# Optimization experiments

Measured on AMD Instinct MI355X. Metric: run time of the kernel, lower is better.

Reference implementation:

```python
import jax, jax.numpy as jnp
import numpy as np
from jax import lax

B, N, D_PTS = 8, 4096, 6
N_POINTS, N_SAMPLES, RADIUS = 1024, 32, 0.2
MLPS = [64, 64, 128]
BN_EPS = 1e-3  # keras BatchNormalization default epsilon


def safe_norm(diff, axis):
    # euclidean norm with a backward-safe sqrt (same forward values)
    sq = jnp.sum(diff * diff, axis=axis)
    pos = sq > 0
    return jnp.where(pos, jnp.sqrt(jnp.where(pos, sq, 1.0)), 0.0)


def setup_inputs() -> dict:
    key = jax.random.key(0)
    ks = jax.random.split(key, 2)
    xyz = jax.random.normal(ks[0], (B, N, 3), jnp.float32)
    points = jax.random.normal(ks[1], (B, N, D_PTS), jnp.float32)
    inp = {"xyz": xyz, "points": points}
    c_in = 3 + D_PTS
    for i, c_out in enumerate(MLPS):
        kw = jax.random.fold_in(key, 100 + i)
        inp[f"w{i}"] = jax.random.normal(kw, (c_in, c_out), jnp.float32) * (1.0 / np.sqrt(c_in))
        inp[f"b{i}"] = jnp.zeros((c_out,), jnp.float32)
        inp[f"g{i}"] = jnp.ones((c_out,), jnp.float32)
        inp[f"be{i}"] = jnp.zeros((c_out,), jnp.float32)
        c_in = c_out
    return inp


def fps(xyz, n_points):
    # farthest point sampling; original seeds with a random index, we use 0 deterministically
    b, n, _ = xyz.shape
    init_idx = jnp.zeros((b,), jnp.int32)
    mask0 = jnp.ones((b, n), xyz.dtype)
    def step(carry, _):
        mask, last = carry
        added = jnp.take_along_axis(xyz, last[:, None, None], axis=1)  # [B,1,D]
        dist = safe_norm(xyz - added, 2) * mask                        # [B,N]
        nxt = jnp.argmax(dist, axis=1).astype(jnp.int32)
        new_mask = jnp.minimum(dist * mask * 1e11, mask)
        return (new_mask, nxt), nxt
    _, ids = lax.scan(step, (mask0, init_idx), None, length=n_points - 1)
    return jnp.concatenate([init_idx[:, None], ids.T], axis=1)  # [B, n_points]


def gather_points(x, idx):
    # x: [B,N,C]; idx: [B,...] -> [B,...,C]
    b = x.shape[0]
    flat = idx.reshape(b, -1)
    out = jnp.take_along_axis(x, flat[..., None], axis=1)
    return out.reshape(idx.shape + (x.shape[-1],))


def query_ball(radius, n_samples, xyz, cent_xyz):
    # faithful to source: compares norm to radius**2 (source quirk), full argsort then slice
    diff = xyz[:, None, :, :] - cent_xyz[:, :, None, :]   # [B,n,N,3]
    dist = safe_norm(diff, 3)                              # [B,n,N]
    dist = jnp.minimum(dist, radius * radius)
    return jnp.argsort(dist, axis=2)[:, :, :n_samples]     # [B,n,n_samples]


def mlp_layer(h, w, b, g, be):
    # pointwise Dense + BatchNormalization (batch stats, axis=-1) + relu
    h = jnp.einsum('bnsc,cd->bnsd', h, w) + b
    mean = jnp.mean(h, axis=(0, 1, 2), keepdims=True)
    var = jnp.var(h, axis=(0, 1, 2), keepdims=True)
    h = g * (h - mean) * lax.rsqrt(var + BN_EPS) + be
    return jax.nn.relu(h)


def forward(xyz, points, params):
    cent_idx = fps(xyz, N_POINTS)                 # [B, n_points]
    cent_xyz = gather_points(xyz, cent_idx)       # [B, n_points, 3]
    group_idx = query_ball(RADIUS, N_SAMPLES, xyz, cent_xyz)  # [B, n_points, n_samples]
    group_xyz = gather_points(xyz, group_idx)     # [B, n_points, n_samples, 3]
    group_pts = gather_points(points, group_idx)  # [B, n_points, n_samples, D]
    h = jnp.concatenate([group_xyz, group_pts], axis=-1)
    for (w, b, g, be) in params:
        h = mlp_layer(h, w, b, g, be)
    return cent_xyz, jnp.max(h, axis=2)           # [B,n_points,3], [B,n_points,128]


def reference(xyz, points, w0, b0, g0, be0, w1, b1, g1, be1, w2, b2, g2, be2):
    params = [(w0, b0, g0, be0), (w1, b1, g1, be1), (w2, b2, g2, be2)]
    return forward(xyz, points, params)
```

## Files before the change

kernel.cpp:

```cpp
#include <hip/hip_runtime.h>

#define NPTS  4096
#define NB    8
#define NC    1024
#define NSAMP 32
#define DP    6
#define C0    9
#define C3    128
#define ROWS_TOT 262144

#define OFF_SS   (32ull<<10)
#define OFF_Y0   (16ull<<20)
#define OFF_Y1   (96ull<<20)
#define OFF_PSUM (168ull<<20)
#define OFF_PSQ  (172ull<<20)
#define OFF_GMX  (176ull<<20)
#define OFF_GMN  (180ull<<20)

typedef unsigned long long ull;
typedef float v2f __attribute__((ext_vector_type(2)));

__device__ __forceinline__ float sqdist_noc(float x, float y, float z,
                                            float cx, float cy, float cz) {
  #pragma clang fp contract(off)
  float dx = x - cx, dy = y - cy, dz = z - cz;
  return dx * dx + dy * dy + dz * dz;
}

template <int CTRL, int RM>
__device__ __forceinline__ float dpp_mov_f(float x) {
  int xi = __float_as_int(x);
  int r = __builtin_amdgcn_update_dpp(xi, xi, CTRL, RM, 0xf, false);
  return __int_as_float(r);
}

__device__ __forceinline__ float wave64_fmax(float x) {
  x = fmaxf(x, dpp_mov_f<0x111, 0xf>(x));
  x = fmaxf(x, dpp_mov_f<0x112, 0xf>(x));
  x = fmaxf(x, dpp_mov_f<0x114, 0xf>(x));
  x = fmaxf(x, dpp_mov_f<0x118, 0xf>(x));
  x = fmaxf(x, dpp_mov_f<0x142, 0xa>(x));
  x = fmaxf(x, dpp_mov_f<0x143, 0xc>(x));
  return x;
}

__global__ __launch_bounds__(256)
void fps_kernel(const float* __restrict__ xyz, float* __restrict__ cent) {
  const int b = blockIdx.x;
  const int t = threadIdx.x;
  const float* X = xyz + (size_t)b * NPTS * 3;
  float* OC = cent + (size_t)b * NC * 3;

  __shared__ float4 sxyz[NPTS];
  __shared__ float4 wkc[2][4];
  __shared__ alignas(16) int wki[2][4];
  __shared__ int sidx[NC];

  for (int p = t; p < NPTS; p += 256)
    sxyz[p] = make_float4(X[p * 3 + 0], X[p * 3 + 1], X[p * 3 + 2], 0.f);
  __syncthreads();

  float px[16], py[16], pz[16], h[16];
  #pragma unroll
  for (int i = 0; i < 16; i++) {
    float4 v = sxyz[t * 16 + i];
    px[i] = v.x; py[i] = v.y; pz[i] = v.z;
    h[i] = fmaf(v.x, v.x, fmaf(v.y, v.y, v.z * v.z));
  }

  const int wv = t >> 6;
  float4 c;

  auto step_body = [&](int pw_) {
    const float c2x = c.x + c.x, c2y = c.y + c.y, c2z = c.z + c.z;
    float key[16]; int idx[16];
    #pragma unroll
    for (int i = 0; i < 16; i++) {
      key[i] = fmaf(pz[i], -c2z, fmaf(py[i], -c2y, fmaf(px[i], -c2x, h[i])));
      idx[i] = i;
    }
    #pragma unroll
    for (int s = 1; s < 16; s <<= 1) {
      #pragma unroll
      for (int i = 0; i < 16; i += 2 * s) {
        bool tk = key[i + s] > key[i];
        key[i] = tk ? key[i + s] : key[i];
        idx[i] = tk ? idx[i + s] : idx[i];
      }
    }
    const float mx = key[0];
    const int mj = idx[0];
    float4 cand = sxyz[(t << 4) + mj];
    float wm = wave64_fmax(mx);
    float smax = __int_as_float(__builtin_amdgcn_readlane(__float_as_int(wm), 63));
    if (mx == smax) {
      wkc[pw_][wv] = make_float4(cand.x, cand.y, cand.z, smax);
      wki[pw_][wv] = (t << 4) + mj;
    }
  };

  auto fold = [&](int pr_) -> int {
    float4 q0 = wkc[pr_][0], q1 = wkc[pr_][1];
    float4 q2 = wkc[pr_][2], q3 = wkc[pr_][3];
    const int4 ii = *(const int4*)&wki[pr_][0];
    bool g1 = q1.w > q0.w; float4 ca = g1 ? q1 : q0; int ia = g1 ? ii.y : ii.x;
    bool g3 = q3.w > q2.w; float4 cb = g3 ? q3 : q2; int ib = g3 ? ii.w : ii.z;
    bool gb = cb.w > ca.w; c = gb ? cb : ca; return gb ? ib : ia;
  };

  if (t == 0) { sidx[0] = 0; h[0] = -__builtin_inff(); }
  c = sxyz[0];
  step_body(1);
  __syncthreads();

  for (int k = 2; k < NC; k++) {
    const int pr = (k - 1) & 1, pw = k & 1;
    int gidx = fold(pr);
    if (t == 0) sidx[k - 1] = gidx;
    if ((gidx >> 4) == t) {
      int m = gidx & 15;
      #pragma unroll
      for (int i = 0; i < 16; i++)
        if (i == m) h[i] = -__builtin_inff();
    }
    step_body(pw);
    __syncthreads();
  }
  {
    int gidx = fold(1023 & 1);
    if (t == 0) sidx[NC - 1] = gidx;
  }
  __syncthreads();
  for (int i = t; i < NC; i += 256) {
    float4 cc = sxyz[sidx[i]];
    OC[i * 3 + 0] = cc.x;
    OC[i * 3 + 1] = cc.y;
    OC[i * 3 + 2] = cc.z;
  }
}

#define BCAP 256
__global__ __launch_bounds__(256)
void ball_dense0_kernel(const float* __restrict__ xyz, const float* __restrict__ pts,
                        const float* __restrict__ cent,
                        const float* __restrict__ W0, const float* __restrict__ b0,
                        float* __restrict__ y0,
                        float* __restrict__ psum, float* __restrict__ psq) {
  const int blk = blockIdx.x;
  const int b = blk >> 10;
  const int t = threadIdx.x;
  const float* X = xyz + (size_t)b * NPTS * 3;
  const float* P = pts + (size_t)b * NPTS * DP;
  const float cx = cent[(size_t)blk * 3 + 0];
  const float cy = cent[(size_t)blk * 3 + 1];
  const float cz = cent[(size_t)blk * 3 + 2];

  __shared__ int scount;
  __shared__ ull skeys[BCAP];
  __shared__ ull ssorted[BCAP];
  __shared__ int sel[NSAMP];
  __shared__ float xs0[NSAMP * C0];
  __shared__ float w0s[C0 * 64];
  __shared__ float b0s[64];
  __shared__ float red[2][NSAMP][64];
  if (t == 0) scount = 0;
  for (int e = t; e < C0 * 64; e += 256) w0s[e] = W0[e];
  if (t < 64) b0s[t] = b0[t];
  __syncthreads();

  {
    float4 xb[12];
    const float4* Xv = (const float4*)(X + (size_t)t * 48);
    #pragma unroll
    for (int i = 0; i < 12; i++) xb[i] = Xv[i];
    const float* xf = (const float*)xb;
    v2f sq2[8];
    {
      #pragma clang fp contract(off)
      const v2f c2x = v2f{cx, cx}, c2y = v2f{cy, cy}, c2z = v2f{cz, cz};
      #pragma unroll
      for (int i = 0; i < 8; i++) {
        v2f x2 = v2f{xf[6 * i + 0], xf[6 * i + 3]};
        v2f y2 = v2f{xf[6 * i + 1], xf[6 * i + 4]};
        v2f z2 = v2f{xf[6 * i + 2], xf[6 * i + 5]};
        v2f dx = x2 - c2x, dy = y2 - c2y, dz = z2 - c2z;
        sq2[i] = (dx * dx + dy * dy) + dz * dz;
      }
    }
    #pragma unroll
    for (int i = 0; i < 16; i++) {
      int j = t * 16 + i;
      float sq = (i & 1) ? sq2[i >> 1].y : sq2[i >> 1].x;
      if (sq < 0.0017f) {
        float d = (sq > 0.f) ? sqrtf(sq) : 0.f;
        if (d < 0.04f) {
          int pos = atomicAdd(&scount, 1);
          if (pos < BCAP)
            skeys[pos] = ((ull)(unsigned)__float_as_int(d) << 12) | (unsigned)j;
        }
      }
    }
  }
  __syncthreads();
  const int M = min(scount, BCAP);

  if (t < M) {
    ull my = skeys[t];
    int r = 0;
    for (int j2 = 0; j2 < M; j2++) r += (skeys[j2] < my);
    ssorted[r] = my;
  }
  __syncthreads();

  if (t < NSAMP) {
    int v;
    if (t < M) {
      v = (int)(ssorted[t] & 0xFFFull);
    } else {
      int s = t - M;
      int idx = s;
      for (int it = 0; it < 40; it++) {
        int c = 0;
        for (int j2 = 0; j2 < M; j2++) c += ((int)(skeys[j2] & 0xFFFull) <= idx);
        int nidx = s + c;
        if (nidx == idx) break;
        idx = nidx;
      }
      v = idx;
    }
    sel[t] = v;
  }
  __syncthreads();

  for (int e = t; e < NSAMP * C0; e += 256) {
    int k = e / C0;
    int cc = e - k * C0;
    int j = sel[k];
    xs0[e] = (cc < 3) ? X[j * 3 + cc] : P[j * DP + (cc - 3)];
  }
  __syncthreads();

  const int row = t >> 3, c8 = (t & 7) * 8;
  float a[8];
  #pragma unroll
  for (int j = 0; j < 8; j++) a[j] = b0s[c8 + j];
  #pragma unroll
  for (int k = 0; k < C0; k++) {
    float xv = xs0[row * C0 + k];
    #pragma unroll
    for (int j = 0; j < 8; j++) a[j] = fmaf(xv, w0s[k * 64 + c8 + j], a[j]);
  }
  float* Y = y0 + ((size_t)blk * NSAMP + row) * 64 + c8;
  *(float4*)(Y + 0) = make_float4(a[0], a[1], a[2], a[3]);
  *(float4*)(Y + 4) = make_float4(a[4], a[5], a[6], a[7]);
  #pragma unroll
  for (int j = 0; j < 8; j++) red[0][row][c8 + j] = a[j];
  #pragma unroll
  for (int j = 0; j < 8; j++) red[1][row][c8 + j] = a[j] * a[j];
  __syncthreads();
  if (t < 64) {
    float S = 0.f, Q = 0.f;
    #pragma unroll
    for (int g = 0; g < NSAMP; g++) { S += red[0][g][t]; Q += red[1][g][t]; }
    psum[(size_t)t * 8192 + blk] = S;
    psq [(size_t)t * 8192 + blk] = Q;
  }
}

__global__ __launch_bounds__(256)
void dense_lane1_kernel(const float* __restrict__ y0, const float* __restrict__ ss0,
                        const float* __restrict__ W1, const float* __restrict__ b1,
                        float* __restrict__ y1,
                        float* __restrict__ psum, float* __restrict__ psq) {
  __shared__ float tr[4][64][33];
  __shared__ float wred[2][4][64];
  const int t = threadIdx.x, wid = t >> 6, lane = t & 63;
  const size_t row = (size_t)blockIdx.x * 256 + (size_t)(wid * 64 + lane);
  float acc[64];
  #pragma unroll
  for (int c = 0; c < 64; c++) acc[c] = b1[c];
  const float* Xr = y0 + row * 64;
  #pragma unroll 1
  for (int k0 = 0; k0 < 64; k0 += 4) {
    float4 xv = *(const float4*)(Xr + k0);
    #pragma unroll
    for (int kk = 0; kk < 4; kk++) {
      const int k = k0 + kk;
      float x = fmaxf(fmaf((&xv.x)[kk], ss0[k], ss0[128 + k]), 0.f);
      const float* Wk = W1 + k * 64;
      #pragma unroll
      for (int c = 0; c < 64; c++) acc[c] = fmaf(x, Wk[c], acc[c]);
    }
  }
  float* Yr = y1 + row * 64;
  #pragma unroll
  for (int c0 = 0; c0 < 64; c0 += 4)
    *(float4*)(Yr + c0) = make_float4(acc[c0], acc[c0 + 1], acc[c0 + 2], acc[c0 + 3]);
  const int c = lane & 31;
  const bool isQ = lane >= 32;
  #pragma unroll
  for (int chunk = 0; chunk < 2; chunk++) {
    __syncthreads();
    #pragma unroll
    for (int j = 0; j < 32; j++) tr[wid][lane][j] = acc[chunk * 32 + j];
    __syncthreads();
    float A = 0.f;
    for (int r = 0; r < 64; r++) {
      float v = tr[wid][r][c];
      A = fmaf(v, isQ ? v : 1.0f, A);
    }
    wred[isQ ? 1 : 0][wid][chunk * 32 + c] = A;
  }
  __syncthreads();
  if (t < 64) {
    float S = 0.f, Q = 0.f;
    #pragma unroll
    for (int w = 0; w < 4; w++) { S += wred[0][w][t]; Q += wred[1][w][t]; }
    psum[(size_t)t * 1024 + blockIdx.x] = S;
    psq [(size_t)t * 1024 + blockIdx.x] = Q;
  }
}

__global__ __launch_bounds__(256)
void dense_lane2_kernel(const float* __restrict__ y1, const float* __restrict__ ss1,
                        const float* __restrict__ W2, const float* __restrict__ b2,
                        float* __restrict__ psum, float* __restrict__ psq,
                        float* __restrict__ gmax, float* __restrict__ gmin) {
  __shared__ float tr[4][64][33];
  __shared__ float wred[2][4][128];
  const int t = threadIdx.x, wid = t >> 6, lane = t & 63;
  const size_t row = (size_t)blockIdx.x * 256 + (size_t)(wid * 64 + lane);
  const int centA = blockIdx.x * 8 + wid * 2;
  const int centB = centA + 1;

  float x[64];
  const float* Xr = y1 + row * 64;
  #pragma unroll
  for (int k0 = 0; k0 < 64; k0 += 4) {
    float4 xv = *(const float4*)(Xr + k0);
    #pragma unroll
    for (int kk = 0; kk < 4; kk++)
      x[k0 + kk] = fmaxf(fmaf((&xv.x)[kk], ss1[k0 + kk], ss1[128 + k0 + kk]), 0.f);
  }

  const int c = lane & 31;
  const bool isQ = lane >= 32;
  #pragma unroll 1
  for (int half = 0; half < 2; half++) {
    float acc[64];
    #pragma unroll
    for (int cc = 0; cc < 64; cc++) acc[cc] = b2[half * 64 + cc];
    #pragma unroll 1
    for (int k = 0; k < 64; k++) {
      const float* Wk = W2 + k * C3 + half * 64;
      const float xk = x[k];
      #pragma unroll
      for (int cc = 0; cc < 64; cc++) acc[cc] = fmaf(xk, Wk[cc], acc[cc]);
    }
    #pragma unroll
    for (int chunk = 0; chunk < 2; chunk++) {
      __syncthreads();
      #pragma unroll
      for (int j = 0; j < 32; j++) tr[wid][lane][j] = acc[chunk * 32 + j];
      __syncthreads();
      const int ch = half * 64 + chunk * 32 + c;
      float A = 0.f, m1 = -__builtin_inff(), m2 = -__builtin_inff();
      for (int r = 0; r < 32; r++) {
        float v = tr[wid][r][c];
        A = fmaf(v, isQ ? v : 1.0f, A);
        m1 = fmaxf(m1, isQ ? -v : v);
      }
      for (int r = 32; r < 64; r++) {
        float v = tr[wid][r][c];
        A = fmaf(v, isQ ? v : 1.0f, A);
        m2 = fmaxf(m2, isQ ? -v : v);
      }
      wred[isQ ? 1 : 0][wid][ch] = A;
      if (!isQ) {
        gmax[(size_t)centA * C3 + ch] = m1;
        gmax[(size_t)centB * C3 + ch] = m2;
      } else {
        gmin[(size_t)centA * C3 + ch] = -m1;
        gmin[(size_t)centB * C3 + ch] = -m2;
      }
    }
  }
  __syncthreads();
  if (t < C3) {
    float S = 0.f, Q = 0.f;
    #pragma unroll
    for (int w = 0; w < 4; w++) { S += wred[0][w][t]; Q += wred[1][w][t]; }
    psum[(size_t)t * 1024 + blockIdx.x] = S;
    psq [(size_t)t * 1024 + blockIdx.x] = Q;
  }
}

template <int NBLK>
__global__ __launch_bounds__(256)
void stats_final_kernel(const float* __restrict__ psum, const float* __restrict__ psq,
                        const float* __restrict__ g, const float* __restrict__ be,
                        float* __restrict__ ss_out) {
  const int c = blockIdx.x, t = threadIdx.x;
  float S = 0.f, Q = 0.f;
  for (int i = t; i < NBLK; i += 256) {
    S += psum[(size_t)c * NBLK + i];
    Q += psq [(size_t)c * NBLK + i];
  }
  __shared__ float sS[256], sQ[256];
  sS[t] = S; sQ[t] = Q;
  __syncthreads();
  #pragma unroll
  for (int off = 128; off; off >>= 1) {
    if (t < off) { sS[t] += sS[t + off]; sQ[t] += sQ[t + off]; }
    __syncthreads();
  }
  if (t == 0) {
    const float inv = 1.0f / 262144.0f;
    float mean = sS[0] * inv;
    float var = sQ[0] * inv - mean * mean;
    float scale = g[c] / sqrtf(var + 1e-3f);
    ss_out[c] = scale;
    ss_out[128 + c] = be[c] - mean * scale;
  }
}

__global__ __launch_bounds__(128)
void pool_final_kernel(const float* __restrict__ gmax, const float* __restrict__ gmin,
                       const float* __restrict__ ss2, float* __restrict__ out1) {
  const int blk = blockIdx.x, c = threadIdx.x;
  const float sc = ss2[c], sh = ss2[128 + c];
  float v = (sc >= 0.f) ? gmax[(size_t)blk * C3 + c] : gmin[(size_t)blk * C3 + c];
  out1[(size_t)blk * C3 + c] = fmaxf(fmaf(v, sc, sh), 0.f);
}

extern "C" void kernel_launch(void* const* d_in, const int* in_sizes, int n_in,
                              void* d_out, int out_size, void* d_ws, size_t ws_size,
                              hipStream_t stream) {
  const float* xyz = (const float*)d_in[0];
  const float* pts = (const float*)d_in[1];
  const float* w0 = (const float*)d_in[2];
  const float* b0 = (const float*)d_in[3];
  const float* g0 = (const float*)d_in[4];
  const float* be0 = (const float*)d_in[5];
  const float* w1 = (const float*)d_in[6];
  const float* b1 = (const float*)d_in[7];
  const float* g1 = (const float*)d_in[8];
  const float* be1 = (const float*)d_in[9];
  const float* w2 = (const float*)d_in[10];
  const float* b2 = (const float*)d_in[11];
  const float* g2 = (const float*)d_in[12];
  const float* be2 = (const float*)d_in[13];

  float* out = (float*)d_out;
  float* cent = out;
  float* out1 = out + (size_t)NB * NC * 3;

  char* ws = (char*)d_ws;
  float* ssA  = (float*)(ws + OFF_SS);
  float* y0   = (float*)(ws + OFF_Y0);
  float* y1   = (float*)(ws + OFF_Y1);
  float* psum = (float*)(ws + OFF_PSUM);
  float* psq  = (float*)(ws + OFF_PSQ);
  float* gmx  = (float*)(ws + OFF_GMX);
  float* gmn  = (float*)(ws + OFF_GMN);

  fps_kernel<<<dim3(NB), dim3(256), 0, stream>>>(xyz, cent);

  ball_dense0_kernel<<<dim3(NB * NC), dim3(256), 0, stream>>>(
      xyz, pts, cent, w0, b0, y0, psum, psq);
  stats_final_kernel<8192><<<dim3(64), dim3(256), 0, stream>>>(psum, psq, g0, be0, ssA + 0 * 256);

  dense_lane1_kernel<<<dim3(ROWS_TOT / 256), dim3(256), 0, stream>>>(
      y0, ssA + 0 * 256, w1, b1, y1, psum, psq);
  stats_final_kernel<1024><<<dim3(64), dim3(256), 0, stream>>>(psum, psq, g1, be1, ssA + 1 * 256);

  dense_lane2_kernel<<<dim3(ROWS_TOT / 256), dim3(256), 0, stream>>>(
      y1, ssA + 1 * 256, w2, b2, psum, psq, gmx, gmn);
  stats_final_kernel<1024><<<dim3(128), dim3(256), 0, stream>>>(psum, psq, g2, be2, ssA + 2 * 256);

  pool_final_kernel<<<dim3(NB * NC), dim3(128), 0, stream>>>(gmx, gmn, ssA + 2 * 256, out1);

  (void)in_sizes; (void)n_in; (void)out_size; (void)ws_size;
}
```

Measured before the change: 807.3 us.

## Fuse FPS and ball-query kernels with progress flags to overlap stages

Merges the farthest-point-sampling kernel and the ball-query/dense0 kernel into one persistent-style launch. Blocks take a ticket from an atomic counter: the first 8 run FPS and publish their progress every 32 centroids through release stores. The remaining blocks spin on that counter and start ball query and the first dense layer for each centroid as soon as it exists. This aims to hide the serial FPS latency behind the ball-query work, at the cost of spin-waiting blocks holding CU slots, an extra memset, and a shared-memory union that may lower occupancy.

```diff
diff --git a/kernel.cpp b/kernel.cpp
--- a/kernel.cpp
+++ b/kernel.cpp
@@ -20,13 +20,6 @@
 typedef unsigned long long ull;
 typedef float v2f __attribute__((ext_vector_type(2)));
 
-__device__ __forceinline__ float sqdist_noc(float x, float y, float z,
-                                            float cx, float cy, float cz) {
-  #pragma clang fp contract(off)
-  float dx = x - cx, dy = y - cy, dz = z - cz;
-  return dx * dx + dy * dy + dz * dz;
-}
-
 template <int CTRL, int RM>
 __device__ __forceinline__ float dpp_mov_f(float x) {
   int xi = __float_as_int(x);
@@ -44,226 +37,254 @@
   return x;
 }
 
+#define BCAP 256
+
+struct FpsShared {
+  float4 sxyz[NPTS];
+  float4 wkc[2][4];
+  int    wki[2][4];
+};
+struct BallShared {
+  ull skeys[BCAP];
+  ull ssorted[BCAP];
+  int sel[NSAMP];
+  float xs0[NSAMP * C0];
+  float w0s[C0 * 64];
+  float b0s[64];
+  float red[2][NSAMP][64];
+  float cbc[4];
+};
+
 __global__ __launch_bounds__(256)
-void fps_kernel(const float* __restrict__ xyz, float* __restrict__ cent) {
-  const int b = blockIdx.x;
+void fps_ball_kernel(const float* __restrict__ xyz, const float* __restrict__ pts,
+                     const float* __restrict__ W0, const float* __restrict__ b0v,
+                     float* __restrict__ cent, float* __restrict__ y0,
+                     float* __restrict__ psum, float* __restrict__ psq,
+                     int* __restrict__ ctl) {
+  __shared__ int s_tk;
+  __shared__ int s_cnt;
+  __shared__ alignas(16) unsigned char smem[sizeof(FpsShared)];
   const int t = threadIdx.x;
-  const float* X = xyz + (size_t)b * NPTS * 3;
-  float* OC = cent + (size_t)b * NC * 3;
-
-  __shared__ float4 sxyz[NPTS];
-  __shared__ float4 wkc[2][4];
-  __shared__ alignas(16) int wki[2][4];
-  __shared__ int sidx[NC];
-
-  for (int p = t; p < NPTS; p += 256)
-    sxyz[p] = make_float4(X[p * 3 + 0], X[p * 3 + 1], X[p * 3 + 2], 0.f);
+  if (t == 0) s_tk = atomicAdd(&ctl[0], 1);
   __syncthreads();
-
-  float px[16], py[16], pz[16], h[16];
-  #pragma unroll
-  for (int i = 0; i < 16; i++) {
-    float4 v = sxyz[t * 16 + i];
-    px[i] = v.x; py[i] = v.y; pz[i] = v.z;
-    h[i] = fmaf(v.x, v.x, fmaf(v.y, v.y, v.z * v.z));
-  }
-
-  const int wv = t >> 6;
-  float4 c;
-
-  auto step_body = [&](int pw_) {
-    const float c2x = c.x + c.x, c2y = c.y + c.y, c2z = c.z + c.z;
-    float key[16]; int idx[16];
+  const int tk = s_tk;
+
+  if (tk < NB) {
+    FpsShared& S = *reinterpret_cast<FpsShared*>(smem);
+    const int b = tk;
+    const float* X = xyz + (size_t)b * NPTS * 3;
+    float* OC = cent + (size_t)b * NC * 3;
+    int* prog = ctl + 16 + 16 * b;
+
+    for (int p = t; p < NPTS; p += 256)
+      S.sxyz[p] = make_float4(X[p * 3 + 0], X[p * 3 + 1], X[p * 3 + 2], 0.f);
+    __syncthreads();
+
+    float px[16], py[16], pz[16], h[16];
     #pragma unroll
     for (int i = 0; i < 16; i++) {
-      key[i] = fmaf(pz[i], -c2z, fmaf(py[i], -c2y, fmaf(px[i], -c2x, h[i])));
-      idx[i] = i;
-    }
-    #pragma unroll
-    for (int s = 1; s < 16; s <<= 1) {
-      #pragma unroll
-      for (int i = 0; i < 16; i += 2 * s) {
-        bool tk = key[i + s] > key[i];
-        key[i] = tk ? key[i + s] : key[i];
-        idx[i] = tk ? idx[i + s] : idx[i];
-      }
-    }
-    const float mx = key[0];
-    const int mj = idx[0];
-    float4 cand = sxyz[(t << 4) + mj];
-    float wm = wave64_fmax(mx);
-    float smax = __int_as_float(__builtin_amdgcn_readlane(__float_as_int(wm), 63));
-    if (mx == smax) {
-      wkc[pw_][wv] = make_float4(cand.x, cand.y, cand.z, smax);
-      wki[pw_][wv] = (t << 4) + mj;
-    }
-  };
-
-  auto fold = [&](int pr_) -> int {
-    float4 q0 = wkc[pr_][0], q1 = wkc[pr_][1];
-    float4 q2 = wkc[pr_][2], q3 = wkc[pr_][3];
-    const int4 ii = *(const int4*)&wki[pr_][0];
-    bool g1 = q1.w > q0.w; float4 ca = g1 ? q1 : q0; int ia = g1 ? ii.y : ii.x;
-    bool g3 = q3.w > q2.w; float4 cb = g3 ? q3 : q2; int ib = g3 ? ii.w : ii.z;
-    bool gb = cb.w > ca.w; c = gb ? cb : ca; return gb ? ib : ia;
-  };
-
-  if (t == 0) { sidx[0] = 0; h[0] = -__builtin_inff(); }
-  c = sxyz[0];
-  step_body(1);
-  __syncthreads();
-
-  for (int k = 2; k < NC; k++) {
-    const int pr = (k - 1) & 1, pw = k & 1;
-    int gidx = fold(pr);
-    if (t == 0) sidx[k - 1] = gidx;
-    if ((gidx >> 4) == t) {
-      int m = gidx & 15;
-      #pragma unroll
-      for (int i = 0; i < 16; i++)
-        if (i == m) h[i] = -__builtin_inff();
-    }
-    step_body(pw);
-    __syncthreads();
-  }
-  {
-    int gidx = fold(1023 & 1);
-    if (t == 0) sidx[NC - 1] = gidx;
-  }
-  __syncthreads();
-  for (int i = t; i < NC; i += 256) {
-    float4 cc = sxyz[sidx[i]];
-    OC[i * 3 + 0] = cc.x;
-    OC[i * 3 + 1] = cc.y;
-    OC[i * 3 + 2] = cc.z;
-  }
-}
-
-#define BCAP 256
-__global__ __launch_bounds__(256)
-void ball_dense0_kernel(const float* __restrict__ xyz, const float* __restrict__ pts,
-                        const float* __restrict__ cent,
-                        const float* __restrict__ W0, const float* __restrict__ b0,
-                        float* __restrict__ y0,
-                        float* __restrict__ psum, float* __restrict__ psq) {
-  const int blk = blockIdx.x;
-  const int b = blk >> 10;
-  const int t = threadIdx.x;
-  const float* X = xyz + (size_t)b * NPTS * 3;
-  const float* P = pts + (size_t)b * NPTS * DP;
-  const float cx = cent[(size_t)blk * 3 + 0];
-  const float cy = cent[(size_t)blk * 3 + 1];
-  const float cz = cent[(size_t)blk * 3 + 2];
-
-  __shared__ int scount;
-  __shared__ ull skeys[BCAP];
-  __shared__ ull ssorted[BCAP];
-  __shared__ int sel[NSAMP];
-  __shared__ float xs0[NSAMP * C0];
-  __shared__ float w0s[C0 * 64];
-  __shared__ float b0s[64];
-  __shared__ float red[2][NSAMP][64];
-  if (t == 0) scount = 0;
-  for (int e = t; e < C0 * 64; e += 256) w0s[e] = W0[e];
-  if (t < 64) b0s[t] = b0[t];
-  __syncthreads();
-
-  {
-    float4 xb[12];
-    const float4* Xv = (const float4*)(X + (size_t)t * 48);
-    #pragma unroll
-    for (int i = 0; i < 12; i++) xb[i] = Xv[i];
-    const float* xf = (const float*)xb;
-    v2f sq2[8];
+      float4 v = S.sxyz[t * 16 + i];
+      px[i] = v.x; py[i] = v.y; pz[i] = v.z;
+      h[i] = fmaf(v.x, v.x, fmaf(v.y, v.y, v.z * v.z));
+    }
+
+    const int wv = t >> 6;
+    float4 c;
+
+    auto step_body = [&](int pw_) {
+      const float c2x = c.x + c.x, c2y = c.y + c.y, c2z = c.z + c.z;
+      float key[16]; int idx[16];
+      #pragma unroll
+      for (int i = 0; i < 16; i++) {
+        key[i] = fmaf(pz[i], -c2z, fmaf(py[i], -c2y, fmaf(px[i], -c2x, h[i])));
+        idx[i] = i;
+      }
+      #pragma unroll
+      for (int s = 1; s < 16; s <<= 1) {
+        #pragma unroll
+        for (int i = 0; i < 16; i += 2 * s) {
+          bool tkn = key[i + s] > key[i];
+          key[i] = tkn ? key[i + s] : key[i];
+          idx[i] = tkn ? idx[i + s] : idx[i];
+        }
+      }
+      const float mx = key[0];
+      const int mj = idx[0];
+      float4 cand = S.sxyz[(t << 4) + mj];
+      float wm = wave64_fmax(mx);
+      float smax = __int_as_float(__builtin_amdgcn_readlane(__float_as_int(wm), 63));
+      if (mx == smax) {
+        S.wkc[pw_][wv] = make_float4(cand.x, cand.y, cand.z, smax);
+        S.wki[pw_][wv] = (t << 4) + mj;
+      }
+    };
+
+    auto fold = [&](int pr_) -> int {
+      float4 q0 = S.wkc[pr_][0], q1 = S.wkc[pr_][1];
+      float4 q2 = S.wkc[pr_][2], q3 = S.wkc[pr_][3];
+      const int4 ii = *(const int4*)&S.wki[pr_][0];
+      bool g1 = q1.w > q0.w; float4 ca = g1 ? q1 : q0; int ia = g1 ? ii.y : ii.x;
+      bool g3 = q3.w > q2.w; float4 cb = g3 ? q3 : q2; int ib = g3 ? ii.w : ii.z;
+      bool gb = cb.w > ca.w; c = gb ? cb : ca; return gb ? ib : ia;
+    };
+
+    c = S.sxyz[0];
+    if (t == 0) {
+      h[0] = -__builtin_inff();
+      OC[0] = c.x; OC[1] = c.y; OC[2] = c.z;
+    }
+    step_body(1);
+    __syncthreads();
+
+    for (int k = 2; k < NC; k++) {
+      const int pr = (k - 1) & 1, pw = k & 1;
+      int gidx = fold(pr);
+      if (t == 0) {
+        OC[(k - 1) * 3 + 0] = c.x;
+        OC[(k - 1) * 3 + 1] = c.y;
+        OC[(k - 1) * 3 + 2] = c.z;
+        if (((k - 1) & 31) == 31)
+          __hip_atomic_store(prog, k, __ATOMIC_RELEASE, __HIP_MEMORY_SCOPE_AGENT);
+      }
+      if ((gidx >> 4) == t) {
+        int m = gidx & 15;
+        #pragma unroll
+        for (int i = 0; i < 16; i++)
+          if (i == m) h[i] = -__builtin_inff();
+      }
+      step_body(pw);
+      __syncthreads();
+    }
     {
-      #pragma clang fp contract(off)
-      const v2f c2x = v2f{cx, cx}, c2y = v2f{cy, cy}, c2z = v2f{cz, cz};
-      #pragma unroll
-      for (int i = 0; i < 8; i++) {
-        v2f x2 = v2f{xf[6 * i + 0], xf[6 * i + 3]};
-        v2f y2 = v2f{xf[6 * i + 1], xf[6 * i + 4]};
-        v2f z2 = v2f{xf[6 * i + 2], xf[6 * i + 5]};
-        v2f dx = x2 - c2x, dy = y2 - c2y, dz = z2 - c2z;
-        sq2[i] = (dx * dx + dy * dy) + dz * dz;
-      }
-    }
-    #pragma unroll
-    for (int i = 0; i < 16; i++) {
-      int j = t * 16 + i;
-      float sq = (i & 1) ? sq2[i >> 1].y : sq2[i >> 1].x;
-      if (sq < 0.0017f) {
-        float d = (sq > 0.f) ? sqrtf(sq) : 0.f;
-        if (d < 0.04f) {
-          int pos = atomicAdd(&scount, 1);
-          if (pos < BCAP)
-            skeys[pos] = ((ull)(unsigned)__float_as_int(d) << 12) | (unsigned)j;
+      fold(1023 & 1);
+      if (t == 0) {
+        OC[1023 * 3 + 0] = c.x;
+        OC[1023 * 3 + 1] = c.y;
+        OC[1023 * 3 + 2] = c.z;
+        __hip_atomic_store(prog, NC, __ATOMIC_RELEASE, __HIP_MEMORY_SCOPE_AGENT);
+      }
+    }
+  } else {
+    BallShared& S = *reinterpret_cast<BallShared*>(smem);
+    const int id = tk - NB;
+    const int cc = id >> 3;
+    const int b = id & 7;
+    const int blk = (b << 10) | cc;
+    const float* X = xyz + (size_t)b * NPTS * 3;
+    const float* P = pts + (size_t)b * NPTS * DP;
+    int* prog = ctl + 16 + 16 * b;
+
+    if (t == 0) s_cnt = 0;
+    for (int e = t; e < C0 * 64; e += 256) S.w0s[e] = W0[e];
+    if (t < 64) S.b0s[t] = b0v[t];
+
+    if (t == 0) {
+      while (__hip_atomic_load(prog, __ATOMIC_ACQUIRE, __HIP_MEMORY_SCOPE_AGENT) < cc + 1)
+        __builtin_amdgcn_s_sleep(32);
+      S.cbc[0] = cent[(size_t)blk * 3 + 0];
+      S.cbc[1] = cent[(size_t)blk * 3 + 1];
+      S.cbc[2] = cent[(size_t)blk * 3 + 2];
+    }
+    __syncthreads();
+    const float cx = S.cbc[0], cy = S.cbc[1], cz = S.cbc[2];
+
+    {
+      float4 xb[12];
+      const float4* Xv = (const float4*)(X + (size_t)t * 48);
+      #pragma unroll
+      for (int i = 0; i < 12; i++) xb[i] = Xv[i];
+      const float* xf = (const float*)xb;
+      v2f sq2[8];
+      {
+        #pragma clang fp contract(off)
+        const v2f c2x = v2f{cx, cx}, c2y = v2f{cy, cy}, c2z = v2f{cz, cz};
+        #pragma unroll
+        for (int i = 0; i < 8; i++) {
+          v2f x2 = v2f{xf[6 * i + 0], xf[6 * i + 3]};
+          v2f y2 = v2f{xf[6 * i + 1], xf[6 * i + 4]};
+          v2f z2 = v2f{xf[6 * i + 2], xf[6 * i + 5]};
+          v2f dx = x2 - c2x, dy = y2 - c2y, dz = z2 - c2z;
+          sq2[i] = (dx * dx + dy * dy) + dz * dz;
         }
       }
-    }
-  }
-  __syncthreads();
-  const int M = min(scount, BCAP);
-
-  if (t < M) {
-    ull my = skeys[t];
-    int r = 0;
-    for (int j2 = 0; j2 < M; j2++) r += (skeys[j2] < my);
-    ssorted[r] = my;
-  }
-  __syncthreads();
-
-  if (t < NSAMP) {
-    int v;
+      #pragma unroll
+      for (int i = 0; i < 16; i++) {
+        int j = t * 16 + i;
+        float sq = (i & 1) ? sq2[i >> 1].y : sq2[i >> 1].x;
+        if (sq < 0.0017f) {
+          float d = (sq > 0.f) ? sqrtf(sq) : 0.f;
+          if (d < 0.04f) {
+            int pos = atomicAdd(&s_cnt, 1);
+            if (pos < BCAP)
+              S.skeys[pos] = ((ull)(unsigned)__float_as_int(d) << 12) | (unsigned)j;
+          }
+        }
+      }
+    }
+    __syncthreads();
+    const int M = min(s_cnt, BCAP);
+
     if (t < M) {
-      v = (int)(ssorted[t] & 0xFFFull);
-    } else {
-      int s = t - M;
-      int idx = s;
-      for (int it = 0; it < 40; it++) {
-        int c = 0;
-        for (int j2 = 0; j2 < M; j2++) c += ((int)(skeys[j2] & 0xFFFull) <= idx);
-        int nidx = s + c;
-        if (nidx == idx) break;
-        idx = nidx;
-      }
-      v = idx;
-    }
-    sel[t] = v;
-  }
-  __syncthreads();
-
-  for (int e = t; e < NSAMP * C0; e += 256) {
-    int k = e / C0;
-    int cc = e - k * C0;
-    int j = sel[k];
-    xs0[e] = (cc < 3) ? X[j * 3 + cc] : P[j * DP + (cc - 3)];
-  }
-  __syncthreads();
-
-  const int row = t >> 3, c8 = (t & 7) * 8;
-  float a[8];
-  #pragma unroll
-  for (int j = 0; j < 8; j++) a[j] = b0s[c8 + j];
-  #pragma unroll
-  for (int k = 0; k < C0; k++) {
-    float xv = xs0[row * C0 + k];
-    #pragma unroll
-    for (int j = 0; j < 8; j++) a[j] = fmaf(xv, w0s[k * 64 + c8 + j], a[j]);
-  }
-  float* Y = y0 + ((size_t)blk * NSAMP + row) * 64 + c8;
-  *(float4*)(Y + 0) = make_float4(a[0], a[1], a[2], a[3]);
-  *(float4*)(Y + 4) = make_float4(a[4], a[5], a[6], a[7]);
-  #pragma unroll
-  for (int j = 0; j < 8; j++) red[0][row][c8 + j] = a[j];
-  #pragma unroll
-  for (int j = 0; j < 8; j++) red[1][row][c8 + j] = a[j] * a[j];
-  __syncthreads();
-  if (t < 64) {
-    float S = 0.f, Q = 0.f;
-    #pragma unroll
-    for (int g = 0; g < NSAMP; g++) { S += red[0][g][t]; Q += red[1][g][t]; }
-    psum[(size_t)t * 8192 + blk] = S;
-    psq [(size_t)t * 8192 + blk] = Q;
+      ull my = S.skeys[t];
+      int r = 0;
+      for (int j2 = 0; j2 < M; j2++) r += (S.skeys[j2] < my);
+      S.ssorted[r] = my;
+    }
+    __syncthreads();
+
+    if (t < NSAMP) {
+      int v;
+      if (t < M) {
+        v = (int)(S.ssorted[t] & 0xFFFull);
+      } else {
+        int s = t - M;
+        int idx = s;
+        for (int it = 0; it < 40; it++) {
+          int cnum = 0;
+          for (int j2 = 0; j2 < M; j2++) cnum += ((int)(S.skeys[j2] & 0xFFFull) <= idx);
+          int nidx = s + cnum;
+          if (nidx == idx) break;
+          idx = nidx;
+        }
+        v = idx;
+      }
+      S.sel[t] = v;
+    }
+    __syncthreads();
+
+    for (int e = t; e < NSAMP * C0; e += 256) {
+      int k = e / C0;
+      int ccc = e - k * C0;
+      int j = S.sel[k];
+      S.xs0[e] = (ccc < 3) ? X[j * 3 + ccc] : P[j * DP + (ccc - 3)];
+    }
+    __syncthreads();
+
+    const int row = t >> 3, c8 = (t & 7) * 8;
+    float a[8];
+    #pragma unroll
+    for (int j = 0; j < 8; j++) a[j] = S.b0s[c8 + j];
+    #pragma unroll
+    for (int k = 0; k < C0; k++) {
+      float xv = S.xs0[row * C0 + k];
+      #pragma unroll
+      for (int j = 0; j < 8; j++) a[j] = fmaf(xv, S.w0s[k * 64 + c8 + j], a[j]);
+    }
+    float* Y = y0 + ((size_t)blk * NSAMP + row) * 64 + c8;
+    *(float4*)(Y + 0) = make_float4(a[0], a[1], a[2], a[3]);
+    *(float4*)(Y + 4) = make_float4(a[4], a[5], a[6], a[7]);
+    #pragma unroll
+    for (int j = 0; j < 8; j++) S.red[0][row][c8 + j] = a[j];
+    #pragma unroll
+    for (int j = 0; j < 8; j++) S.red[1][row][c8 + j] = a[j] * a[j];
+    __syncthreads();
+    if (t < 64) {
+      float Ss = 0.f, Q = 0.f;
+      #pragma unroll
+      for (int g = 0; g < NSAMP; g++) { Ss += S.red[0][g][t]; Q += S.red[1][g][t]; }
+      psum[(size_t)t * 8192 + blk] = Ss;
+      psq [(size_t)t * 8192 + blk] = Q;
+    }
   }
 }
 
@@ -456,6 +477,7 @@
   float* out1 = out + (size_t)NB * NC * 3;
 
   char* ws = (char*)d_ws;
+  int*   ctl  = (int*)ws;
   float* ssA  = (float*)(ws + OFF_SS);
   float* y0   = (float*)(ws + OFF_Y0);
   float* y1   = (float*)(ws + OFF_Y1);
@@ -464,10 +486,10 @@
   float* gmx  = (float*)(ws + OFF_GMX);
   float* gmn  = (float*)(ws + OFF_GMN);
 
-  fps_kernel<<<dim3(NB), dim3(256), 0, stream>>>(xyz, cent);
-
-  ball_dense0_kernel<<<dim3(NB * NC), dim3(256), 0, stream>>>(
-      xyz, pts, cent, w0, b0, y0, psum, psq);
+  hipMemsetAsync(ctl, 0, 1024, stream);
+
+  fps_ball_kernel<<<dim3(NB + NB * NC), dim3(256), 0, stream>>>(
+      xyz, pts, w0, b0, cent, y0, psum, psq, ctl);
   stats_final_kernel<8192><<<dim3(64), dim3(256), 0, stream>>>(psum, psq, g0, be0, ssA + 0 * 256);
 
   dense_lane1_kernel<<<dim3(ROWS_TOT / 256), dim3(256), 0, stream>>>(
```

Result: slower. 915.2 us (+13.4%).
